# Kernel tuning notes

Hardware: AMD Instinct MI355X
Metric: run time of the kernel (lower is better)

Reference implementation:

```python
import jax, jax.numpy as jnp
import numpy as np

N_NODES = 50000
N_EDGES = 200000
IN_FEATS = 32
OUT_FEATS = 32
EDGE_DIM = 16


def setup_inputs() -> dict:
    key = jax.random.key(0)
    k1, k2, k3, k4, k5 = jax.random.split(key, 5)
    feat = jax.random.normal(k1, (N_NODES, IN_FEATS), dtype=jnp.float32)
    efeat = jax.random.normal(k2, (N_EDGES, EDGE_DIM), dtype=jnp.float32)
    src = jax.random.randint(k3, (N_EDGES,), 0, N_NODES, dtype=jnp.int32)
    dst = jax.random.randint(k4, (N_EDGES,), 0, N_NODES, dtype=jnp.int32)
    # edge_func = Linear(EDGE_DIM -> IN_FEATS*OUT_FEATS)
    W_edge = jax.random.normal(k5, (EDGE_DIM, IN_FEATS * OUT_FEATS), dtype=jnp.float32) * (1.0 / np.sqrt(EDGE_DIM))
    b_edge = jnp.zeros((IN_FEATS * OUT_FEATS,), dtype=jnp.float32)
    bias = jnp.zeros((OUT_FEATS,), dtype=jnp.float32)
    return {"feat": feat, "efeat": efeat, "src": src, "dst": dst,
            "W_edge": W_edge, "b_edge": b_edge, "bias": bias}


def reference(feat, efeat, src, dst, W_edge, b_edge, bias):
    # edge_func: (E, edge_dim) -> (E, in, out) edge-conditioned weights
    w = (efeat @ W_edge + b_edge).reshape(-1, IN_FEATS, OUT_FEATS)
    # u_mul_e + sum over in dim  ==  per-edge matvec: h_src[e] @ W[e]
    h_src = feat[src]                               # (E, in) gather
    msg = jnp.einsum('ei,eio->eo', h_src, w)        # (E, out)
    # mean reduce over incoming edges per destination node
    agg = jax.ops.segment_sum(msg, dst, num_segments=N_NODES)   # (N, out)
    deg = jax.ops.segment_sum(jnp.ones((msg.shape[0],), dtype=msg.dtype), dst,
                              num_segments=N_NODES)
    agg = agg / jnp.maximum(deg, 1.0)[:, None]      # zero-degree nodes stay 0
    return agg + bias
```

## Files before the change

### kernel.cpp

```cpp
#include <hip/hip_runtime.h>
#include <hip/hip_bf16.h>

#define NNODES 50000
#define NEDGES 200000
#define WCT_ROW 552
#define WCT_BYTES (32 * WCT_ROW * 2)
#define HROW 40
#define TILE_EDGES 64
#define NTILES (NEDGES / TILE_EDGES)
#define CHAIN_BLKS ((NEDGES + 255) / 256)
#define DROW 33

#define MSG_OFF   0
#define HEAD_OFF  25600000
#define NEXT_OFF  25800000
#define WCT_OFF   26600000

using f32x4 = __attribute__((ext_vector_type(4))) float;
using f16x2 = __attribute__((ext_vector_type(2))) _Float16;
using f16x4 = __attribute__((ext_vector_type(4))) _Float16;
using f16x8 = __attribute__((ext_vector_type(8))) _Float16;

__device__ __forceinline__ f16x2 pkrtz(float a, float b) {
    return __builtin_bit_cast(f16x2, __builtin_amdgcn_cvt_pkrtz(a, b));
}

__device__ __forceinline__ void gload_lds16(const void* g, void* l) {
    __builtin_amdgcn_global_load_lds(
        (const __attribute__((address_space(1))) unsigned int*)g,
        (__attribute__((address_space(3))) unsigned int*)l, 16, 0, 0);
}

#define WCT_BLKS 69
__global__ void init_kernel(const float* __restrict__ W_edge,
                            const float* __restrict__ b_edge,
                            _Float16* __restrict__ wct,
                            unsigned* __restrict__ head) {
    int b = blockIdx.x;
    if (b < WCT_BLKS) {
        int gid = b * 256 + threadIdx.x;
        if (gid >= 32 * WCT_ROW) return;
        int n = gid / WCT_ROW;
        int c = gid - n * WCT_ROW;
        float v = 0.0f;
        if (c < 512)      v = W_edge[(c & 15) * 1024 + (c >> 4) * 32 + n];
        else if (c < 544) v = b_edge[(c - 512) * 32 + n];
        wct[gid] = (_Float16)v;
    } else {
        int gid = (b - WCT_BLKS) * 256 + threadIdx.x;
        if (gid < NNODES) head[gid] = 0xFFFFFFFFu;
    }
}

__global__ __launch_bounds__(256, 3) void work_kernel(
    const float* __restrict__ feat, const float* __restrict__ efeat,
    const int* __restrict__ src, const int* __restrict__ dst,
    const _Float16* __restrict__ wct_g,
    float4* __restrict__ msg4, unsigned* __restrict__ head,
    unsigned* __restrict__ next) {

    __shared__ __align__(16) unsigned short wct_lds[32 * WCT_ROW];
    __shared__ __align__(16) unsigned short h_lds[TILE_EDGES * HROW];
    __shared__ __align__(16) float dtile[TILE_EDGES * DROW];

    const int t = threadIdx.x;

    if (blockIdx.x >= NTILES) {
        int e = (blockIdx.x - NTILES) * 256 + t;
        if (e < NEDGES)
            next[e] = atomicExch(&head[dst[e]], (unsigned)e);
        return;
    }

    const int lane = t & 63;
    const int wave = t >> 6;
    const int ebase = blockIdx.x * TILE_EDGES;

    {
        const char* gsrc = (const char*)wct_g;
        char* lbase = (char*)wct_lds;
        #pragma unroll
        for (int c = 0; c < 9; ++c) {
            int chunk = wave + c * 4;
            if (chunk < 35) {
                int boff = (chunk << 10) + lane * 16;
                if (boff < WCT_BYTES) gload_lds16(gsrc + boff, lbase + boff);
            }
        }
    }

    {
        int et = t >> 2, p = t & 3;
        int se = src[ebase + et];
        const float* fp = feat + se * 32 + p * 8;
        float4 a = *(const float4*)fp;
        float4 b = *(const float4*)(fp + 4);
        uint4 hp;
        hp.x = __builtin_bit_cast(unsigned int, pkrtz(a.x, a.y));
        hp.y = __builtin_bit_cast(unsigned int, pkrtz(a.z, a.w));
        hp.z = __builtin_bit_cast(unsigned int, pkrtz(b.x, b.y));
        hp.w = __builtin_bit_cast(unsigned int, pkrtz(b.z, b.w));
        *(uint4*)(void*)(h_lds + et * HROW + p * 8) = hp;
    }

    const int r16 = lane & 15;
    const int g   = lane >> 4;
    const int wbase = wave * 16;
    const int eg = ebase + wbase + r16;

    const float* efp = efeat + eg * 16 + (g & 1) * 8;
    float4 e0 = *(const float4*)efp;
    float4 e1 = *(const float4*)(efp + 4);
    f16x2 ef2[4] = { pkrtz(e0.x, e0.y), pkrtz(e0.z, e0.w),
                     pkrtz(e1.x, e1.y), pkrtz(e1.z, e1.w) };

    __syncthreads();

    unsigned int hbc[16];
    f16x8 af_bias;
    {
        const uint4* hrow = (const uint4*)(void*)(h_lds + (wbase + r16) * HROW);
        unsigned int hw[16];
        #pragma unroll
        for (int q = 0; q < 4; ++q) {
            uint4 v = hrow[q];
            hw[q*4+0] = v.x; hw[q*4+1] = v.y; hw[q*4+2] = v.z; hw[q*4+3] = v.w;
        }
        const bool hi = (g >> 1) & 1;
        #pragma unroll
        for (int s = 0; s < 16; ++s) {
            unsigned int x = hi ? (hw[s] >> 16) : (hw[s] & 0xffffu);
            hbc[s] = x | (x << 16);
        }
        af_bias = *(const f16x8*)(void*)((const _Float16*)h_lds + (wbase + r16) * HROW + g * 8);
    }

    const _Float16* brow0 = (const _Float16*)wct_lds + r16 * WCT_ROW;
    const _Float16* brow1 = (const _Float16*)wct_lds + (16 + r16) * WCT_ROW;

    f32x4 acc0 = {0.f, 0.f, 0.f, 0.f};
    f32x4 acc1 = {0.f, 0.f, 0.f, 0.f};

    #pragma unroll
    for (int s = 0; s < 16; ++s) {
        const int koff = s * 32 + g * 8;
        f16x8 b0 = *(const f16x8*)(brow0 + koff);
        f16x8 b1 = *(const f16x8*)(brow1 + koff);
        f16x2 hb = __builtin_bit_cast(f16x2, hbc[s]);
        f16x2 p0 = hb * ef2[0], p1 = hb * ef2[1], p2 = hb * ef2[2], p3 = hb * ef2[3];
        f16x4 lo  = __builtin_shufflevector(p0, p1, 0, 1, 2, 3);
        f16x4 hi4 = __builtin_shufflevector(p2, p3, 0, 1, 2, 3);
        f16x8 af  = __builtin_shufflevector(lo, hi4, 0, 1, 2, 3, 4, 5, 6, 7);
        acc0 = __builtin_amdgcn_mfma_f32_16x16x32_f16(af, b0, acc0, 0, 0, 0);
        acc1 = __builtin_amdgcn_mfma_f32_16x16x32_f16(af, b1, acc1, 0, 0, 0);
    }
    {
        const int koff = 512 + g * 8;
        f16x8 b0 = *(const f16x8*)(brow0 + koff);
        f16x8 b1 = *(const f16x8*)(brow1 + koff);
        acc0 = __builtin_amdgcn_mfma_f32_16x16x32_f16(af_bias, b0, acc0, 0, 0, 0);
        acc1 = __builtin_amdgcn_mfma_f32_16x16x32_f16(af_bias, b1, acc1, 0, 0, 0);
    }

    {
        const int browD = wbase + g * 4;
        #pragma unroll
        for (int r = 0; r < 4; ++r) {
            dtile[(browD + r) * DROW + r16]      = acc0[r];
            dtile[(browD + r) * DROW + 16 + r16] = acc1[r];
        }
    }
    asm volatile("s_waitcnt lgkmcnt(0)" ::: "memory");
    __builtin_amdgcn_sched_barrier(0);

    {
        const int rA = wbase + (lane >> 3);
        const int cA = (lane & 7) * 4;
        float4 vA = *(const float4*)(dtile + rA * DROW + cA);
        float4 vB = *(const float4*)(dtile + (rA + 8) * DROW + cA);
        float4* mp = msg4 + (size_t)blockIdx.x * 512 + wave * 128;
        mp[lane]      = vA;
        mp[64 + lane] = vB;
    }
}

__global__ __launch_bounds__(256) void pull_kernel(
    const float4* __restrict__ msg4, const unsigned* __restrict__ head,
    const unsigned* __restrict__ next, const float* __restrict__ bias,
    float* __restrict__ out) {

    int gid = blockIdx.x * 256 + threadIdx.x;
    if (gid >= NNODES * 8) return;
    int n = gid >> 3, Q = gid & 7;

    float4 s = {0.f, 0.f, 0.f, 0.f};
    float degf = 0.0f;

    unsigned e = head[n];
    while (e != 0xFFFFFFFFu) {
        float4 m = msg4[(size_t)e * 8 + Q];
        s.x += m.x; s.y += m.y; s.z += m.z; s.w += m.w;
        degf += 1.0f;
        e = next[e];
    }

    float inv = 1.0f / fmaxf(degf, 1.0f);
    float4 b = ((const float4*)bias)[Q];
    float4 o = { s.x * inv + b.x, s.y * inv + b.y, s.z * inv + b.z, s.w * inv + b.w };
    *(float4*)(out + n * 32 + Q * 4) = o;
}

extern "C" void kernel_launch(void* const* d_in, const int* in_sizes, int n_in,
                              void* d_out, int out_size, void* d_ws, size_t ws_size,
                              hipStream_t stream) {
    const float* feat   = (const float*)d_in[0];
    const float* efeat  = (const float*)d_in[1];
    const int*   src    = (const int*)d_in[2];
    const int*   dst    = (const int*)d_in[3];
    const float* W_edge = (const float*)d_in[4];
    const float* b_edge = (const float*)d_in[5];
    const float* bias   = (const float*)d_in[6];

    char* ws = (char*)d_ws;
    float4*   msg4 = (float4*)(ws + MSG_OFF);
    unsigned* head = (unsigned*)(ws + HEAD_OFF);
    unsigned* next = (unsigned*)(ws + NEXT_OFF);
    _Float16* wct  = (_Float16*)(ws + WCT_OFF);
    float*    out  = (float*)d_out;

    init_kernel<<<WCT_BLKS + (NNODES + 255) / 256, 256, 0, stream>>>(
        W_edge, b_edge, wct, head);
    work_kernel<<<NTILES + CHAIN_BLKS, 256, 0, stream>>>(
        feat, efeat, src, dst, wct, msg4, head, next);
    pull_kernel<<<(NNODES * 8 + 255) / 256, 256, 0, stream>>>(
        msg4, head, next, bias, out);
}
```

Before: 42.78 us.

## Process two edge tiles per block to amortize W staging and prefetch

Each GEMM block now handles two consecutive 64-edge tiles, loading the shared edge-weight matrix into LDS once for both. Source indices, edge features and the second tile's node features are loaded early so they overlap the first tile's MFMA work. This halves the number of GEMM blocks and the total LDS staging traffic, at the cost of higher register pressure and less block-level parallelism.

```diff
diff --git a/kernel.cpp b/kernel.cpp
--- a/kernel.cpp
+++ b/kernel.cpp
@@ -8,6 +8,7 @@
 #define HROW 40
 #define TILE_EDGES 64
 #define NTILES (NEDGES / TILE_EDGES)
+#define GEMM_BLOCKS ((NTILES + 1) / 2)
 #define CHAIN_BLKS ((NEDGES + 255) / 256)
 #define DROW 33
 
@@ -65,8 +66,8 @@
 
     const int t = threadIdx.x;
 
-    if (blockIdx.x >= NTILES) {
-        int e = (blockIdx.x - NTILES) * 256 + t;
+    if (blockIdx.x >= GEMM_BLOCKS) {
+        int e = (blockIdx.x - GEMM_BLOCKS) * 256 + t;
         if (e < NEDGES)
             next[e] = atomicExch(&head[dst[e]], (unsigned)e);
         return;
@@ -74,7 +75,16 @@
 
     const int lane = t & 63;
     const int wave = t >> 6;
-    const int ebase = blockIdx.x * TILE_EDGES;
+    const int tile0 = blockIdx.x * 2;
+    const int tile1 = tile0 + 1;
+    const bool has1 = (tile1 < NTILES);
+    const int ebase0 = tile0 * TILE_EDGES;
+    const int ebase1 = tile1 * TILE_EDGES;
+
+    const int r16 = lane & 15;
+    const int g   = lane >> 4;
+    const int wbase = wave * 16;
+    const int et = t >> 2, p = t & 3;
 
     {
         const char* gsrc = (const char*)wct_g;
@@ -89,10 +99,24 @@
         }
     }
 
-    {
-        int et = t >> 2, p = t & 3;
-        int se = src[ebase + et];
-        const float* fp = feat + se * 32 + p * 8;
+    const int se0 = src[ebase0 + et];
+    int se1 = 0;
+    if (has1) se1 = src[ebase1 + et];
+
+    float4 ef0a, ef0b, ef1a, ef1b;
+    {
+        const float* efp = efeat + (ebase0 + wbase + r16) * 16 + (g & 1) * 8;
+        ef0a = *(const float4*)efp;
+        ef0b = *(const float4*)(efp + 4);
+    }
+    if (has1) {
+        const float* efp = efeat + (ebase1 + wbase + r16) * 16 + (g & 1) * 8;
+        ef1a = *(const float4*)efp;
+        ef1b = *(const float4*)(efp + 4);
+    }
+
+    {
+        const float* fp = feat + se0 * 32 + p * 8;
         float4 a = *(const float4*)fp;
         float4 b = *(const float4*)(fp + 4);
         uint4 hp;
@@ -103,18 +127,13 @@
         *(uint4*)(void*)(h_lds + et * HROW + p * 8) = hp;
     }
 
-    const int r16 = lane & 15;
-    const int g   = lane >> 4;
-    const int wbase = wave * 16;
-    const int eg = ebase + wbase + r16;
-
-    const float* efp = efeat + eg * 16 + (g & 1) * 8;
-    float4 e0 = *(const float4*)efp;
-    float4 e1 = *(const float4*)(efp + 4);
-    f16x2 ef2[4] = { pkrtz(e0.x, e0.y), pkrtz(e0.z, e0.w),
-                     pkrtz(e1.x, e1.y), pkrtz(e1.z, e1.w) };
+    f16x2 ef2[4] = { pkrtz(ef0a.x, ef0a.y), pkrtz(ef0a.z, ef0a.w),
+                     pkrtz(ef0b.x, ef0b.y), pkrtz(ef0b.z, ef0b.w) };
 
     __syncthreads();
+
+    const _Float16* brow0 = (const _Float16*)wct_lds + r16 * WCT_ROW;
+    const _Float16* brow1 = (const _Float16*)wct_lds + (16 + r16) * WCT_ROW;
 
     unsigned int hbc[16];
     f16x8 af_bias;
@@ -135,8 +154,12 @@
         af_bias = *(const f16x8*)(void*)((const _Float16*)h_lds + (wbase + r16) * HROW + g * 8);
     }
 
-    const _Float16* brow0 = (const _Float16*)wct_lds + r16 * WCT_ROW;
-    const _Float16* brow1 = (const _Float16*)wct_lds + (16 + r16) * WCT_ROW;
+    float4 f1a = {0,0,0,0}, f1b = {0,0,0,0};
+    if (has1) {
+        const float* fp = feat + se1 * 32 + p * 8;
+        f1a = *(const float4*)fp;
+        f1b = *(const float4*)(fp + 4);
+    }
 
     f32x4 acc0 = {0.f, 0.f, 0.f, 0.f};
     f32x4 acc1 = {0.f, 0.f, 0.f, 0.f};
@@ -172,13 +195,89 @@
     }
     asm volatile("s_waitcnt lgkmcnt(0)" ::: "memory");
     __builtin_amdgcn_sched_barrier(0);
-
     {
         const int rA = wbase + (lane >> 3);
         const int cA = (lane & 7) * 4;
         float4 vA = *(const float4*)(dtile + rA * DROW + cA);
         float4 vB = *(const float4*)(dtile + (rA + 8) * DROW + cA);
-        float4* mp = msg4 + (size_t)blockIdx.x * 512 + wave * 128;
+        float4* mp = msg4 + (size_t)ebase0 * 8 + wave * 128;
+        mp[lane]      = vA;
+        mp[64 + lane] = vB;
+    }
+
+    if (!has1) return;
+
+    {
+        uint4 hp;
+        hp.x = __builtin_bit_cast(unsigned int, pkrtz(f1a.x, f1a.y));
+        hp.y = __builtin_bit_cast(unsigned int, pkrtz(f1a.z, f1a.w));
+        hp.z = __builtin_bit_cast(unsigned int, pkrtz(f1b.x, f1b.y));
+        hp.w = __builtin_bit_cast(unsigned int, pkrtz(f1b.z, f1b.w));
+        *(uint4*)(void*)(h_lds + et * HROW + p * 8) = hp;
+    }
+    asm volatile("s_waitcnt lgkmcnt(0)" ::: "memory");
+    __builtin_amdgcn_sched_barrier(0);
+
+    ef2[0] = pkrtz(ef1a.x, ef1a.y); ef2[1] = pkrtz(ef1a.z, ef1a.w);
+    ef2[2] = pkrtz(ef1b.x, ef1b.y); ef2[3] = pkrtz(ef1b.z, ef1b.w);
+
+    {
+        const uint4* hrow = (const uint4*)(void*)(h_lds + (wbase + r16) * HROW);
+        unsigned int hw[16];
+        #pragma unroll
+        for (int q = 0; q < 4; ++q) {
+            uint4 v = hrow[q];
+            hw[q*4+0] = v.x; hw[q*4+1] = v.y; hw[q*4+2] = v.z; hw[q*4+3] = v.w;
+        }
+        const bool hi = (g >> 1) & 1;
+        #pragma unroll
+        for (int s = 0; s < 16; ++s) {
+            unsigned int x = hi ? (hw[s] >> 16) : (hw[s] & 0xffffu);
+            hbc[s] = x | (x << 16);
+        }
+        af_bias = *(const f16x8*)(void*)((const _Float16*)h_lds + (wbase + r16) * HROW + g * 8);
+    }
+
+    acc0 = (f32x4){0.f, 0.f, 0.f, 0.f};
+    acc1 = (f32x4){0.f, 0.f, 0.f, 0.f};
+
+    #pragma unroll
+    for (int s = 0; s < 16; ++s) {
+        const int koff = s * 32 + g * 8;
+        f16x8 b0 = *(const f16x8*)(brow0 + koff);
+        f16x8 b1 = *(const f16x8*)(brow1 + koff);
+        f16x2 hb = __builtin_bit_cast(f16x2, hbc[s]);
+        f16x2 p0 = hb * ef2[0], p1 = hb * ef2[1], p2 = hb * ef2[2], p3 = hb * ef2[3];
+        f16x4 lo  = __builtin_shufflevector(p0, p1, 0, 1, 2, 3);
+        f16x4 hi4 = __builtin_shufflevector(p2, p3, 0, 1, 2, 3);
+        f16x8 af  = __builtin_shufflevector(lo, hi4, 0, 1, 2, 3, 4, 5, 6, 7);
+        acc0 = __builtin_amdgcn_mfma_f32_16x16x32_f16(af, b0, acc0, 0, 0, 0);
+        acc1 = __builtin_amdgcn_mfma_f32_16x16x32_f16(af, b1, acc1, 0, 0, 0);
+    }
+    {
+        const int koff = 512 + g * 8;
+        f16x8 b0 = *(const f16x8*)(brow0 + koff);
+        f16x8 b1 = *(const f16x8*)(brow1 + koff);
+        acc0 = __builtin_amdgcn_mfma_f32_16x16x32_f16(af_bias, b0, acc0, 0, 0, 0);
+        acc1 = __builtin_amdgcn_mfma_f32_16x16x32_f16(af_bias, b1, acc1, 0, 0, 0);
+    }
+
+    {
+        const int browD = wbase + g * 4;
+        #pragma unroll
+        for (int r = 0; r < 4; ++r) {
+            dtile[(browD + r) * DROW + r16]      = acc0[r];
+            dtile[(browD + r) * DROW + 16 + r16] = acc1[r];
+        }
+    }
+    asm volatile("s_waitcnt lgkmcnt(0)" ::: "memory");
+    __builtin_amdgcn_sched_barrier(0);
+    {
+        const int rA = wbase + (lane >> 3);
+        const int cA = (lane & 7) * 4;
+        float4 vA = *(const float4*)(dtile + rA * DROW + cA);
+        float4 vB = *(const float4*)(dtile + (rA + 8) * DROW + cA);
+        float4* mp = msg4 + (size_t)ebase1 * 8 + wave * 128;
         mp[lane]      = vA;
         mp[64 + lane] = vB;
     }
@@ -230,7 +329,7 @@
 
     init_kernel<<<WCT_BLKS + (NNODES + 255) / 256, 256, 0, stream>>>(
         W_edge, b_edge, wct, head);
-    work_kernel<<<NTILES + CHAIN_BLKS, 256, 0, stream>>>(
+    work_kernel<<<GEMM_BLOCKS + CHAIN_BLKS, 256, 0, stream>>>(
         feat, efeat, src, dst, wct, msg4, head, next);
     pull_kernel<<<(NNODES * 8 + 255) / 256, 256, 0, stream>>>(
         msg4, head, next, bias, out);
```

Result: faster. 40.82 us (-4.6%).
